# Optimization experiments

Measured on AMD Instinct MI355X. Metric: run time of the kernel, lower is better.

## Reference

```python
import jax, jax.numpy as jnp
import numpy as np

N_NODES = 50000
N_EDGES = 800000
NFEAT = 128
NHID = 128
NCLASS = 10
NUM_GRAPHS = 512


def setup_inputs() -> dict:
    key = jax.random.key(0)
    ks = jax.random.split(key, 8)
    node_feat = jax.random.normal(ks[0], (N_NODES, NFEAT), dtype=jnp.float32)
    W1 = jax.random.normal(ks[1], (NFEAT, NHID), dtype=jnp.float32) * (1.0 / np.sqrt(NFEAT))
    W2 = jax.random.normal(ks[2], (NHID, NHID), dtype=jnp.float32) * (1.0 / np.sqrt(NHID))
    mlp_w = jax.random.normal(ks[3], (NHID, NCLASS), dtype=jnp.float32) * (1.0 / np.sqrt(NHID))
    mlp_b = jnp.zeros((NCLASS,), dtype=jnp.float32)
    edge_src = jax.random.randint(ks[4], (N_EDGES,), 0, N_NODES, dtype=jnp.int32)
    edge_dst = jax.random.randint(ks[5], (N_EDGES,), 0, N_NODES, dtype=jnp.int32)
    graph_ids = jnp.sort(jax.random.randint(ks[6], (N_NODES,), 0, NUM_GRAPHS, dtype=jnp.int32))
    return {"node_feat": node_feat, "W1": W1, "W2": W2, "mlp_w": mlp_w,
            "mlp_b": mlp_b, "edge_src": edge_src, "edge_dst": edge_dst,
            "graph_ids": graph_ids}


def reference(node_feat, W1, W2, mlp_w, mlp_b, edge_src, edge_dst, graph_ids):
    # node_degs: in-degree + 1 (self loop), as used by GraphConvolution's normalization
    ones_e = jnp.ones((N_EDGES,), dtype=node_feat.dtype)
    deg = jax.ops.segment_sum(ones_e, edge_dst, num_segments=N_NODES) + 1.0  # [N]

    def gconv(x, W):
        h = x @ W                                                     # [N, H]
        msg = jax.ops.segment_sum(h[edge_src], edge_dst, num_segments=N_NODES)
        return (h + msg) / deg[:, None]                               # mean over self + neighbors

    x = jax.nn.relu(gconv(node_feat, W1))
    x = gconv(x, W2)                                                  # [N, NHID]

    # per-graph mean readout (the Python loop over graph_sizes == segment mean)
    counts = jax.ops.segment_sum(jnp.ones((N_NODES,), x.dtype), graph_ids,
                                 num_segments=NUM_GRAPHS)             # [G]
    gsum = jax.ops.segment_sum(x, graph_ids, num_segments=NUM_GRAPHS)  # [G, NHID]
    gmean = gsum / jnp.maximum(counts, 1.0)[:, None]

    logits = gmean @ mlp_w + mlp_b                                    # [G, NCLASS]
    return jax.nn.log_softmax(logits, axis=1)
```

## Files before the change

### kernel.cpp

```cpp
#include <hip/hip_runtime.h>

#define N_NODES 50000
#define N_EDGES 800000
#define NFEAT 128
#define NHID 128
#define NCLASS 10
#define NUM_GRAPHS 512
#define GEMM_BLOCKS 782
#define SLOT 64
#define NSLICE 6250

#define G1_GEMM 782
#define G1_BKT 1024
#define G1_GRID (G1_GEMM + G1_BKT)

typedef __attribute__((ext_vector_type(8))) short bf16x8;
typedef __attribute__((ext_vector_type(4))) float f32x4;

__device__ inline ushort f2bf(float f) {
  union { float f; uint u; } c; c.f = f;
  return (ushort)((c.u + 0x7fffu + ((c.u >> 16) & 1u)) >> 16);
}
__device__ inline float bf2f_lo(uint u) { union { uint u; float f; } c; c.u = u << 16; return c.f; }
__device__ inline float bf2f_hi(uint u) { union { uint u; float f; } c; c.u = u & 0xffff0000u; return c.f; }
__device__ inline float bf2f_s(ushort h) { union { uint u; float f; } c; c.u = ((uint)h) << 16; return c.f; }

template <bool XFP32>
__device__ inline void gemm_body(const void* __restrict__ Xv,
                                 const ushort* __restrict__ Wp,
                                 ushort* __restrict__ Y,
                                 ushort* xs, ushort* wsh,
                                 int base, int tid) {
  const int rem = N_NODES - base;
  for (int i = tid; i < 2048; i += 256)
    ((uint4*)wsh)[i] = ((const uint4*)Wp)[i];

  for (int g = tid; g < 1024; g += 256) {
    int row = g >> 4;
    int k0 = (g & 15) << 3;
    int wt = row >> 4, ks = k0 >> 5;
    int lane = (row & 15) + (((k0 >> 3) & 3) << 4);
    uint4 v;
    if (row < rem) {
      if (XFP32) {
        const float* s = (const float*)Xv + (size_t)(base + row) * 128 + k0;
        float4 p0 = ((const float4*)s)[0];
        float4 p1 = ((const float4*)s)[1];
        v.x = (uint)f2bf(p0.x) | ((uint)f2bf(p0.y) << 16);
        v.y = (uint)f2bf(p0.z) | ((uint)f2bf(p0.w) << 16);
        v.z = (uint)f2bf(p1.x) | ((uint)f2bf(p1.y) << 16);
        v.w = (uint)f2bf(p1.z) | ((uint)f2bf(p1.w) << 16);
      } else {
        v = *(const uint4*)((const ushort*)Xv + (size_t)(base + row) * 128 + k0);
      }
    } else {
      v.x = 0; v.y = 0; v.z = 0; v.w = 0;
    }
    *(uint4*)&xs[((((wt << 2) + ks) << 6) + lane) << 3] = v;
  }
  __syncthreads();

  const int wave = tid >> 6, lane = tid & 63;
  f32x4 acc[8];
#pragma unroll
  for (int i = 0; i < 8; ++i) acc[i] = f32x4{0.f, 0.f, 0.f, 0.f};
  bf16x8 a[4];
#pragma unroll
  for (int ks = 0; ks < 4; ++ks)
    a[ks] = *(const bf16x8*)&xs[((((wave << 2) + ks) << 6) + lane) << 3];
#pragma unroll
  for (int ks = 0; ks < 4; ++ks) {
#pragma unroll
    for (int nt = 0; nt < 8; ++nt) {
      bf16x8 b = *(const bf16x8*)&wsh[((((nt << 2) + ks) << 6) + lane) << 3];
      acc[nt] = __builtin_amdgcn_mfma_f32_16x16x32_bf16(a[ks], b, acc[nt], 0, 0, 0);
    }
  }
  const int r0 = base + wave * 16 + ((lane >> 4) << 2);
  const int c0 = lane & 15;
#pragma unroll
  for (int nt = 0; nt < 8; ++nt)
#pragma unroll
    for (int r = 0; r < 4; ++r) {
      int row = r0 + r;
      if (row < N_NODES)
        Y[(size_t)row * 128 + (nt << 4) + c0] = f2bf(acc[nt][r]);
    }
}

__global__ __launch_bounds__(256) void k_wpack(const float* __restrict__ W1,
                                               const float* __restrict__ W2,
                                               ushort* __restrict__ wp1,
                                               ushort* __restrict__ wp2) {
  int idx = blockIdx.x * 256 + threadIdx.x;
  const float* W = (idx < 16384) ? W1 : W2;
  ushort* op = (idx < 16384) ? wp1 : wp2;
  int j = idx & 16383;
  int lane = (j >> 3) & 63;
  int e = j & 7;
  int frag = j >> 9;
  int nt = frag >> 2, ks = frag & 3;
  int c = nt * 16 + (lane & 15);
  int k = ks * 32 + (lane >> 4) * 8 + e;
  op[j] = f2bf(W[k * 128 + c]);
}

__global__ __launch_bounds__(256) void k_fused1(const float* __restrict__ feat,
                                                const ushort* __restrict__ wp1,
                                                const int* __restrict__ esrc,
                                                const int* __restrict__ edst,
                                                int* __restrict__ cnt,
                                                ushort* __restrict__ csr16,
                                                ushort* __restrict__ Y) {
  __shared__ ushort xs[4 * 4 * 64 * 8];
  __shared__ ushort wsh[32 * 64 * 8];
  const int b = blockIdx.x;
  const int tid = threadIdx.x;
  if (b < G1_GEMM) {
    gemm_body<true>(feat, wp1, Y, xs, wsh, b * 64, tid);
  } else {
    const int g = b & 7;
    const int m = (b - G1_GEMM) >> 3;
    const int lo = g * NSLICE, hi = lo + NSLICE;
    for (int e = m * 256 + tid; e < N_EDGES; e += 128 * 256) {
      int d = edst[e];
      if (d >= lo && d < hi) {
        int p = atomicAdd(&cnt[d], 1);
        if (p < SLOT) csr16[(size_t)d * SLOT + p] = (ushort)esrc[e];
      }
    }
  }
}

__device__ inline void unpack_add(uint2 u, float4& a) {
  a.x += bf2f_lo(u.x); a.y += bf2f_hi(u.x);
  a.z += bf2f_lo(u.y); a.w += bf2f_hi(u.y);
}

__device__ inline float4 gather_sum(const uint2* __restrict__ Hv,
                                    const ushort* __restrict__ nb,
                                    int deg, int q) {
  float4 a = {0.f, 0.f, 0.f, 0.f};
  int e = 0;
  for (; e + 8 <= deg; e += 8) {
    uint4 iv = *(const uint4*)(nb + e);
    uint2 u0 = Hv[(size_t)(iv.x & 0xffffu) * 32 + q];
    uint2 u1 = Hv[(size_t)(iv.x >> 16) * 32 + q];
    uint2 u2 = Hv[(size_t)(iv.y & 0xffffu) * 32 + q];
    uint2 u3 = Hv[(size_t)(iv.y >> 16) * 32 + q];
    uint2 u4 = Hv[(size_t)(iv.z & 0xffffu) * 32 + q];
    uint2 u5 = Hv[(size_t)(iv.z >> 16) * 32 + q];
    uint2 u6 = Hv[(size_t)(iv.w & 0xffffu) * 32 + q];
    uint2 u7 = Hv[(size_t)(iv.w >> 16) * 32 + q];
    unpack_add(u0, a); unpack_add(u1, a); unpack_add(u2, a); unpack_add(u3, a);
    unpack_add(u4, a); unpack_add(u5, a); unpack_add(u6, a); unpack_add(u7, a);
  }
  if (e + 4 <= deg) {
    uint2 iv = *(const uint2*)(nb + e);
    uint2 u0 = Hv[(size_t)(iv.x & 0xffffu) * 32 + q];
    uint2 u1 = Hv[(size_t)(iv.x >> 16) * 32 + q];
    uint2 u2 = Hv[(size_t)(iv.y & 0xffffu) * 32 + q];
    uint2 u3 = Hv[(size_t)(iv.y >> 16) * 32 + q];
    unpack_add(u0, a); unpack_add(u1, a); unpack_add(u2, a); unpack_add(u3, a);
    e += 4;
  }
  for (; e < deg; ++e) {
    uint2 u = Hv[(size_t)nb[e] * 32 + q];
    unpack_add(u, a);
  }
  return a;
}

__global__ __launch_bounds__(256) void k_agg1(const ushort* __restrict__ H,
                                              const ushort* __restrict__ csr16,
                                              const int* __restrict__ cnt,
                                              ushort* __restrict__ Out) {
  const int w = threadIdx.x >> 6;
  const int l = threadIdx.x & 63;
  const int h = l >> 5, q = l & 31;
  const int node = blockIdx.x * 8 + w * 2 + h;
  const int deg = min(cnt[node], SLOT);
  const ushort* nb = csr16 + (size_t)node * SLOT;
  const uint2* __restrict__ Hv = (const uint2*)H;
  float4 a = gather_sum(Hv, nb, deg, q);
  uint2 uh = Hv[(size_t)node * 32 + q];
  float inv = 1.0f / (float)(deg + 1);
  float r0 = fmaxf((bf2f_lo(uh.x) + a.x) * inv, 0.f);
  float r1 = fmaxf((bf2f_hi(uh.x) + a.y) * inv, 0.f);
  float r2 = fmaxf((bf2f_lo(uh.y) + a.z) * inv, 0.f);
  float r3 = fmaxf((bf2f_hi(uh.y) + a.w) * inv, 0.f);
  uint2 ov;
  ov.x = (uint)f2bf(r0) | ((uint)f2bf(r1) << 16);
  ov.y = (uint)f2bf(r2) | ((uint)f2bf(r3) << 16);
  ((uint2*)Out)[(size_t)node * 32 + q] = ov;
}

__global__ __launch_bounds__(256) void k_gemm2(const ushort* __restrict__ X,
                                               const ushort* __restrict__ Wp,
                                               ushort* __restrict__ Y) {
  __shared__ ushort xs[4 * 4 * 64 * 8];
  __shared__ ushort wsh[32 * 64 * 8];
  gemm_body<false>(X, Wp, Y, xs, wsh, blockIdx.x * 64, threadIdx.x);
}

__global__ __launch_bounds__(256) void k_agg_ro(const ushort* __restrict__ H,
                                                const ushort* __restrict__ csr16,
                                                const int* __restrict__ cnt,
                                                const int* __restrict__ gid,
                                                float* __restrict__ gsum,
                                                float* __restrict__ gcnt) {
  __shared__ float rows[8][128];
  __shared__ int gids[8];
  const int w = threadIdx.x >> 6;
  const int l = threadIdx.x & 63;
  const int h = l >> 5, q = l & 31;
  const int slot = w * 2 + h;
  const int node = blockIdx.x * 8 + slot;
  const int deg = min(cnt[node], SLOT);
  const ushort* nb = csr16 + (size_t)node * SLOT;
  const uint2* __restrict__ Hv = (const uint2*)H;
  float4 a = gather_sum(Hv, nb, deg, q);
  uint2 uh = Hv[(size_t)node * 32 + q];
  float inv = 1.0f / (float)(deg + 1);
  float4 rr;
  rr.x = bf2f_s(f2bf((bf2f_lo(uh.x) + a.x) * inv));
  rr.y = bf2f_s(f2bf((bf2f_hi(uh.x) + a.y) * inv));
  rr.z = bf2f_s(f2bf((bf2f_lo(uh.y) + a.z) * inv));
  rr.w = bf2f_s(f2bf((bf2f_hi(uh.y) + a.w) * inv));
  *(float4*)&rows[slot][q * 4] = rr;
  if (q == 0) gids[slot] = gid[node];
  __syncthreads();
  const int t = threadIdx.x;
  if (t < 128) {
    float acc = rows[0][t];
    int g = gids[0];
#pragma unroll
    for (int r = 1; r < 8; ++r) {
      int gr = gids[r];
      if (gr != g) {
        atomicAdd(&gsum[g * 128 + t], acc);
        acc = 0.f;
        g = gr;
      }
      acc += rows[r][t];
    }
    atomicAdd(&gsum[g * 128 + t], acc);
  } else if (t == 128) {
    float c = 1.f;
    int g = gids[0];
#pragma unroll
    for (int r = 1; r < 8; ++r) {
      int gr = gids[r];
      if (gr != g) {
        atomicAdd(&gcnt[g], c);
        c = 0.f;
        g = gr;
      }
      c += 1.f;
    }
    atomicAdd(&gcnt[g], c);
  }
}

__global__ __launch_bounds__(128) void k_mlp(const float* __restrict__ gsum,
                                             const float* __restrict__ gcnt,
                                             const float* __restrict__ Wm,
                                             const float* __restrict__ bm,
                                             float* __restrict__ out) {
  __shared__ float m[128];
  __shared__ float lg[NCLASS];
  const int g = blockIdx.x;
  const int t = threadIdx.x;
  float cnt = fmaxf(gcnt[g], 1.0f);
  m[t] = gsum[g * 128 + t] / cnt;
  __syncthreads();
  if (t < NCLASS) {
    float s = bm[t];
#pragma unroll
    for (int k = 0; k < 128; ++k) s += m[k] * Wm[k * NCLASS + t];
    lg[t] = s;
  }
  __syncthreads();
  if (t < NCLASS) {
    float mx = lg[0];
#pragma unroll
    for (int i = 1; i < NCLASS; ++i) mx = fmaxf(mx, lg[i]);
    float sum = 0.f;
#pragma unroll
    for (int i = 0; i < NCLASS; ++i) sum += expf(lg[i] - mx);
    out[g * NCLASS + t] = lg[t] - mx - logf(sum);
  }
}

extern "C" void kernel_launch(void* const* d_in, const int* in_sizes, int n_in,
                              void* d_out, int out_size, void* d_ws, size_t ws_size,
                              hipStream_t stream) {
  const float* feat = (const float*)d_in[0];
  const float* W1   = (const float*)d_in[1];
  const float* W2   = (const float*)d_in[2];
  const float* Wm   = (const float*)d_in[3];
  const float* bm   = (const float*)d_in[4];
  const int* esrc   = (const int*)d_in[5];
  const int* edst   = (const int*)d_in[6];
  const int* gid    = (const int*)d_in[7];
  float* out = (float*)d_out;

  int* cnt      = (int*)d_ws;
  ushort* csr16 = (ushort*)(cnt + 50048);
  ushort* wp1   = csr16 + (size_t)N_NODES * SLOT;
  ushort* wp2   = wp1 + 16384;
  ushort* bufA  = wp2 + 16384;
  ushort* bufB  = bufA + (size_t)N_NODES * NHID;
  float* gsum   = (float*)(bufB + (size_t)N_NODES * NHID);
  float* gcnt   = gsum + NUM_GRAPHS * NHID;

  hipMemsetAsync(cnt, 0, (size_t)50048 * sizeof(int), stream);
  hipMemsetAsync(gsum, 0, (size_t)(NUM_GRAPHS * NHID + 512) * sizeof(float), stream);

  k_wpack<<<128, 256, 0, stream>>>(W1, W2, wp1, wp2);

  k_fused1<<<G1_GRID, 256, 0, stream>>>(feat, wp1, esrc, edst, cnt, csr16, bufA);

  k_agg1<<<N_NODES / 8, 256, 0, stream>>>(bufA, csr16, cnt, bufB);

  k_gemm2<<<GEMM_BLOCKS, 256, 0, stream>>>(bufB, wp2, bufA);

  k_agg_ro<<<N_NODES / 8, 256, 0, stream>>>(bufA, csr16, cnt, gid, gsum, gcnt);

  k_mlp<<<NUM_GRAPHS, 128, 0, stream>>>(gsum, gcnt, Wm, bm, out);
}
```

Baseline: 232.1 us.

## Bucket edges by XCC id with dynamic tickets and widen gather loads to 16B

The edge-bucketing blocks now choose their destination slice from the hardware XCC id, so the cnt/csr atomics for a slice stay on one chiplet's L2. Work is handed out as chunks of edges through per-slice atomic tickets, one wave at a time, in place of a fixed block stride. The aggregation kernels switch from 8-byte to 16-byte gathers, with 16 lanes per node and 16 nodes per block, so each neighbour row takes fewer load instructions. The XCC scheme assumes blocks spread evenly across the 8 XCCs. A slice whose XCC gets few bucket blocks will finish late.

```diff
diff --git a/kernel.cpp b/kernel.cpp
--- a/kernel.cpp
+++ b/kernel.cpp
@@ -9,6 +9,8 @@
 #define GEMM_BLOCKS 782
 #define SLOT 64
 #define NSLICE 6250
+#define BKT_CHUNK 3125
+#define BKT_NCHUNK 256
 
 #define G1_GEMM 782
 #define G1_BKT 1024
@@ -110,6 +112,7 @@
                                                 const int* __restrict__ esrc,
                                                 const int* __restrict__ edst,
                                                 int* __restrict__ cnt,
+                                                int* __restrict__ ticket,
                                                 ushort* __restrict__ csr16,
                                                 ushort* __restrict__ Y) {
   __shared__ ushort xs[4 * 4 * 64 * 8];
@@ -119,80 +122,97 @@
   if (b < G1_GEMM) {
     gemm_body<true>(feat, wp1, Y, xs, wsh, b * 64, tid);
   } else {
-    const int g = b & 7;
-    const int m = (b - G1_GEMM) >> 3;
+    uint xcc;
+    asm volatile("s_getreg_b32 %0, hwreg(HW_REG_XCC_ID)" : "=s"(xcc));
+    const int g = (int)(xcc & 7);
     const int lo = g * NSLICE, hi = lo + NSLICE;
-    for (int e = m * 256 + tid; e < N_EDGES; e += 128 * 256) {
-      int d = edst[e];
-      if (d >= lo && d < hi) {
-        int p = atomicAdd(&cnt[d], 1);
-        if (p < SLOT) csr16[(size_t)d * SLOT + p] = (ushort)esrc[e];
+    const int lane = tid & 63;
+    for (;;) {
+      int c = 0;
+      if (lane == 0) c = atomicAdd(&ticket[g], 1);
+      c = __shfl(c, 0);
+      if (c >= BKT_NCHUNK) break;
+      const int e0 = c * BKT_CHUNK, e1 = e0 + BKT_CHUNK;
+      for (int e = e0 + lane; e < e1; e += 64) {
+        int d = edst[e];
+        if (d >= lo && d < hi) {
+          int p = atomicAdd(&cnt[d], 1);
+          if (p < SLOT) csr16[(size_t)d * SLOT + p] = (ushort)esrc[e];
+        }
       }
     }
   }
 }
 
-__device__ inline void unpack_add(uint2 u, float4& a) {
-  a.x += bf2f_lo(u.x); a.y += bf2f_hi(u.x);
-  a.z += bf2f_lo(u.y); a.w += bf2f_hi(u.y);
-}
-
-__device__ inline float4 gather_sum(const uint2* __restrict__ Hv,
-                                    const ushort* __restrict__ nb,
-                                    int deg, int q) {
-  float4 a = {0.f, 0.f, 0.f, 0.f};
+__device__ inline void unpack_add(uint4 u, float4& a0, float4& a1) {
+  a0.x += bf2f_lo(u.x); a0.y += bf2f_hi(u.x);
+  a0.z += bf2f_lo(u.y); a0.w += bf2f_hi(u.y);
+  a1.x += bf2f_lo(u.z); a1.y += bf2f_hi(u.z);
+  a1.z += bf2f_lo(u.w); a1.w += bf2f_hi(u.w);
+}
+
+__device__ inline void gather_sum(const uint4* __restrict__ Hv,
+                                  const ushort* __restrict__ nb,
+                                  int deg, int q, float4& a0, float4& a1) {
   int e = 0;
   for (; e + 8 <= deg; e += 8) {
     uint4 iv = *(const uint4*)(nb + e);
-    uint2 u0 = Hv[(size_t)(iv.x & 0xffffu) * 32 + q];
-    uint2 u1 = Hv[(size_t)(iv.x >> 16) * 32 + q];
-    uint2 u2 = Hv[(size_t)(iv.y & 0xffffu) * 32 + q];
-    uint2 u3 = Hv[(size_t)(iv.y >> 16) * 32 + q];
-    uint2 u4 = Hv[(size_t)(iv.z & 0xffffu) * 32 + q];
-    uint2 u5 = Hv[(size_t)(iv.z >> 16) * 32 + q];
-    uint2 u6 = Hv[(size_t)(iv.w & 0xffffu) * 32 + q];
-    uint2 u7 = Hv[(size_t)(iv.w >> 16) * 32 + q];
-    unpack_add(u0, a); unpack_add(u1, a); unpack_add(u2, a); unpack_add(u3, a);
-    unpack_add(u4, a); unpack_add(u5, a); unpack_add(u6, a); unpack_add(u7, a);
+    uint4 u0 = Hv[(size_t)(iv.x & 0xffffu) * 16 + q];
+    uint4 u1 = Hv[(size_t)(iv.x >> 16) * 16 + q];
+    uint4 u2 = Hv[(size_t)(iv.y & 0xffffu) * 16 + q];
+    uint4 u3 = Hv[(size_t)(iv.y >> 16) * 16 + q];
+    uint4 u4 = Hv[(size_t)(iv.z & 0xffffu) * 16 + q];
+    uint4 u5 = Hv[(size_t)(iv.z >> 16) * 16 + q];
+    uint4 u6 = Hv[(size_t)(iv.w & 0xffffu) * 16 + q];
+    uint4 u7 = Hv[(size_t)(iv.w >> 16) * 16 + q];
+    unpack_add(u0, a0, a1); unpack_add(u1, a0, a1);
+    unpack_add(u2, a0, a1); unpack_add(u3, a0, a1);
+    unpack_add(u4, a0, a1); unpack_add(u5, a0, a1);
+    unpack_add(u6, a0, a1); unpack_add(u7, a0, a1);
   }
   if (e + 4 <= deg) {
     uint2 iv = *(const uint2*)(nb + e);
-    uint2 u0 = Hv[(size_t)(iv.x & 0xffffu) * 32 + q];
-    uint2 u1 = Hv[(size_t)(iv.x >> 16) * 32 + q];
-    uint2 u2 = Hv[(size_t)(iv.y & 0xffffu) * 32 + q];
-    uint2 u3 = Hv[(size_t)(iv.y >> 16) * 32 + q];
-    unpack_add(u0, a); unpack_add(u1, a); unpack_add(u2, a); unpack_add(u3, a);
+    uint4 u0 = Hv[(size_t)(iv.x & 0xffffu) * 16 + q];
+    uint4 u1 = Hv[(size_t)(iv.x >> 16) * 16 + q];
+    uint4 u2 = Hv[(size_t)(iv.y & 0xffffu) * 16 + q];
+    uint4 u3 = Hv[(size_t)(iv.y >> 16) * 16 + q];
+    unpack_add(u0, a0, a1); unpack_add(u1, a0, a1);
+    unpack_add(u2, a0, a1); unpack_add(u3, a0, a1);
     e += 4;
   }
   for (; e < deg; ++e) {
-    uint2 u = Hv[(size_t)nb[e] * 32 + q];
-    unpack_add(u, a);
-  }
-  return a;
+    uint4 u = Hv[(size_t)nb[e] * 16 + q];
+    unpack_add(u, a0, a1);
+  }
 }
 
 __global__ __launch_bounds__(256) void k_agg1(const ushort* __restrict__ H,
                                               const ushort* __restrict__ csr16,
                                               const int* __restrict__ cnt,
                                               ushort* __restrict__ Out) {
-  const int w = threadIdx.x >> 6;
-  const int l = threadIdx.x & 63;
-  const int h = l >> 5, q = l & 31;
-  const int node = blockIdx.x * 8 + w * 2 + h;
+  const int q = threadIdx.x & 15;
+  const int node = blockIdx.x * 16 + (threadIdx.x >> 4);
   const int deg = min(cnt[node], SLOT);
   const ushort* nb = csr16 + (size_t)node * SLOT;
-  const uint2* __restrict__ Hv = (const uint2*)H;
-  float4 a = gather_sum(Hv, nb, deg, q);
-  uint2 uh = Hv[(size_t)node * 32 + q];
+  const uint4* __restrict__ Hv = (const uint4*)H;
+  float4 a0 = {0.f, 0.f, 0.f, 0.f}, a1 = {0.f, 0.f, 0.f, 0.f};
+  gather_sum(Hv, nb, deg, q, a0, a1);
+  uint4 uh = Hv[(size_t)node * 16 + q];
   float inv = 1.0f / (float)(deg + 1);
-  float r0 = fmaxf((bf2f_lo(uh.x) + a.x) * inv, 0.f);
-  float r1 = fmaxf((bf2f_hi(uh.x) + a.y) * inv, 0.f);
-  float r2 = fmaxf((bf2f_lo(uh.y) + a.z) * inv, 0.f);
-  float r3 = fmaxf((bf2f_hi(uh.y) + a.w) * inv, 0.f);
-  uint2 ov;
-  ov.x = (uint)f2bf(r0) | ((uint)f2bf(r1) << 16);
-  ov.y = (uint)f2bf(r2) | ((uint)f2bf(r3) << 16);
-  ((uint2*)Out)[(size_t)node * 32 + q] = ov;
+  float v0 = fmaxf((bf2f_lo(uh.x) + a0.x) * inv, 0.f);
+  float v1 = fmaxf((bf2f_hi(uh.x) + a0.y) * inv, 0.f);
+  float v2 = fmaxf((bf2f_lo(uh.y) + a0.z) * inv, 0.f);
+  float v3 = fmaxf((bf2f_hi(uh.y) + a0.w) * inv, 0.f);
+  float v4 = fmaxf((bf2f_lo(uh.z) + a1.x) * inv, 0.f);
+  float v5 = fmaxf((bf2f_hi(uh.z) + a1.y) * inv, 0.f);
+  float v6 = fmaxf((bf2f_lo(uh.w) + a1.z) * inv, 0.f);
+  float v7 = fmaxf((bf2f_hi(uh.w) + a1.w) * inv, 0.f);
+  uint4 ov;
+  ov.x = (uint)f2bf(v0) | ((uint)f2bf(v1) << 16);
+  ov.y = (uint)f2bf(v2) | ((uint)f2bf(v3) << 16);
+  ov.z = (uint)f2bf(v4) | ((uint)f2bf(v5) << 16);
+  ov.w = (uint)f2bf(v6) | ((uint)f2bf(v7) << 16);
+  ((uint4*)Out)[(size_t)node * 16 + q] = ov;
 }
 
 __global__ __launch_bounds__(256) void k_gemm2(const ushort* __restrict__ X,
@@ -209,25 +229,29 @@
                                                 const int* __restrict__ gid,
                                                 float* __restrict__ gsum,
                                                 float* __restrict__ gcnt) {
-  __shared__ float rows[8][128];
-  __shared__ int gids[8];
-  const int w = threadIdx.x >> 6;
-  const int l = threadIdx.x & 63;
-  const int h = l >> 5, q = l & 31;
-  const int slot = w * 2 + h;
-  const int node = blockIdx.x * 8 + slot;
+  __shared__ float rows[16][128];
+  __shared__ int gids[16];
+  const int q = threadIdx.x & 15;
+  const int slot = threadIdx.x >> 4;
+  const int node = blockIdx.x * 16 + slot;
   const int deg = min(cnt[node], SLOT);
   const ushort* nb = csr16 + (size_t)node * SLOT;
-  const uint2* __restrict__ Hv = (const uint2*)H;
-  float4 a = gather_sum(Hv, nb, deg, q);
-  uint2 uh = Hv[(size_t)node * 32 + q];
+  const uint4* __restrict__ Hv = (const uint4*)H;
+  float4 a0 = {0.f, 0.f, 0.f, 0.f}, a1 = {0.f, 0.f, 0.f, 0.f};
+  gather_sum(Hv, nb, deg, q, a0, a1);
+  uint4 uh = Hv[(size_t)node * 16 + q];
   float inv = 1.0f / (float)(deg + 1);
-  float4 rr;
-  rr.x = bf2f_s(f2bf((bf2f_lo(uh.x) + a.x) * inv));
-  rr.y = bf2f_s(f2bf((bf2f_hi(uh.x) + a.y) * inv));
-  rr.z = bf2f_s(f2bf((bf2f_lo(uh.y) + a.z) * inv));
-  rr.w = bf2f_s(f2bf((bf2f_hi(uh.y) + a.w) * inv));
-  *(float4*)&rows[slot][q * 4] = rr;
+  float4 r0, r1;
+  r0.x = bf2f_s(f2bf((bf2f_lo(uh.x) + a0.x) * inv));
+  r0.y = bf2f_s(f2bf((bf2f_hi(uh.x) + a0.y) * inv));
+  r0.z = bf2f_s(f2bf((bf2f_lo(uh.y) + a0.z) * inv));
+  r0.w = bf2f_s(f2bf((bf2f_hi(uh.y) + a0.w) * inv));
+  r1.x = bf2f_s(f2bf((bf2f_lo(uh.z) + a1.x) * inv));
+  r1.y = bf2f_s(f2bf((bf2f_hi(uh.z) + a1.y) * inv));
+  r1.z = bf2f_s(f2bf((bf2f_lo(uh.w) + a1.z) * inv));
+  r1.w = bf2f_s(f2bf((bf2f_hi(uh.w) + a1.w) * inv));
+  *(float4*)&rows[slot][q * 8] = r0;
+  *(float4*)&rows[slot][q * 8 + 4] = r1;
   if (q == 0) gids[slot] = gid[node];
   __syncthreads();
   const int t = threadIdx.x;
@@ -235,7 +259,7 @@
     float acc = rows[0][t];
     int g = gids[0];
 #pragma unroll
-    for (int r = 1; r < 8; ++r) {
+    for (int r = 1; r < 16; ++r) {
       int gr = gids[r];
       if (gr != g) {
         atomicAdd(&gsum[g * 128 + t], acc);
@@ -249,7 +273,7 @@
     float c = 1.f;
     int g = gids[0];
 #pragma unroll
-    for (int r = 1; r < 8; ++r) {
+    for (int r = 1; r < 16; ++r) {
       int gr = gids[r];
       if (gr != g) {
         atomicAdd(&gcnt[g], c);
@@ -306,7 +330,8 @@
   float* out = (float*)d_out;
 
   int* cnt      = (int*)d_ws;
-  ushort* csr16 = (ushort*)(cnt + 50048);
+  int* ticket   = cnt + 50048;
+  ushort* csr16 = (ushort*)(ticket + 64);
   ushort* wp1   = csr16 + (size_t)N_NODES * SLOT;
   ushort* wp2   = wp1 + 16384;
   ushort* bufA  = wp2 + 16384;
@@ -314,18 +339,18 @@
   float* gsum   = (float*)(bufB + (size_t)N_NODES * NHID);
   float* gcnt   = gsum + NUM_GRAPHS * NHID;
 
-  hipMemsetAsync(cnt, 0, (size_t)50048 * sizeof(int), stream);
+  hipMemsetAsync(cnt, 0, (size_t)(50048 + 64) * sizeof(int), stream);
   hipMemsetAsync(gsum, 0, (size_t)(NUM_GRAPHS * NHID + 512) * sizeof(float), stream);
 
   k_wpack<<<128, 256, 0, stream>>>(W1, W2, wp1, wp2);
 
-  k_fused1<<<G1_GRID, 256, 0, stream>>>(feat, wp1, esrc, edst, cnt, csr16, bufA);
-
-  k_agg1<<<N_NODES / 8, 256, 0, stream>>>(bufA, csr16, cnt, bufB);
+  k_fused1<<<G1_GRID, 256, 0, stream>>>(feat, wp1, esrc, edst, cnt, ticket, csr16, bufA);
+
+  k_agg1<<<N_NODES / 16, 256, 0, stream>>>(bufA, csr16, cnt, bufB);
 
   k_gemm2<<<GEMM_BLOCKS, 256, 0, stream>>>(bufB, wp2, bufA);
 
-  k_agg_ro<<<N_NODES / 8, 256, 0, stream>>>(bufA, csr16, cnt, gid, gsum, gcnt);
+  k_agg_ro<<<N_NODES / 16, 256, 0, stream>>>(bufA, csr16, cnt, gid, gsum, gcnt);
 
   k_mlp<<<NUM_GRAPHS, 128, 0, stream>>>(gsum, gcnt, Wm, bm, out);
 }
```

After: 287.0 us. 1.24x slower.
